# Kernel tuning notes

Measured on AMD Instinct MI355X. Metric: run time of the kernel, lower is better.

## Reference

```python
import jax, jax.numpy as jnp
import numpy as np

B, NR, NT, NUM_ITER = 8192, 128, 64, 64


def setup_inputs() -> dict:
    key = jax.random.key(0)
    k1, k2, k3, k4 = jax.random.split(key, 4)
    Ht = jax.random.normal(k1, (B, NR, NT), dtype=jnp.float32) / np.sqrt(NR)
    yt = jax.random.normal(k2, (B, NR), dtype=jnp.float32)
    sigmat0 = jax.random.uniform(k3, (B,), dtype=jnp.float32) * 0.5 + 0.05
    # prior probabilities alpha[:,0] after slicing; keep strictly in (0,1)
    alpha = 0.2 + 0.6 * jax.random.uniform(k4, (NT,), dtype=jnp.float32)
    taui = jnp.ones((NUM_ITER,), dtype=jnp.float32)   # per-layer taui weights
    delta = jnp.full((NUM_ITER,), 0.1, dtype=jnp.float32)  # per-layer step sizes
    return {"yt": yt, "Ht": Ht, "sigmat0": sigmat0, "alpha": alpha,
            "taui": taui, "delta": delta}


def _cmd_step(s, c, HH, yH, sig2, taui_i, delta_i, t_x):
    # t_x is the temperature used inside tanh for xt (1.0 on the first layer,
    # |taui_i| otherwise); grad_x always uses |taui_i| as in the original code.
    taui_abs = jnp.abs(taui_i)
    xt = jnp.tanh((c + s) * 0.5 * t_x)                      # [B, NT]
    xHH = jnp.einsum('bn,bnm->bm', xt, HH)                  # [B, NT]
    grad_L = sig2 * jnp.tanh(s * 0.5) + 0.5 * taui_abs * (1.0 - xt ** 2) * (xHH - yH)
    return s - delta_i * grad_L


def reference(yt, Ht, sigmat0, alpha, taui, delta):
    # Precompute Gram matrix and matched filter output
    HH = jnp.einsum('brn,brm->bnm', Ht, Ht)                 # [B, NT, NT]
    yH = jnp.einsum('br,brn->bn', yt, Ht)                   # [B, NT]
    c = jnp.log(1.0 / alpha - 1.0)                          # [NT], prior offset
    sig2 = (sigmat0 ** 2)[:, None]                          # [B, 1]
    s0 = jnp.zeros_like(yH)                                 # [B, NT]

    # first layer: xt temperature fixed to 1 (first_iter=True)
    s = _cmd_step(s0, c, HH, yH, sig2, taui[0], delta[0], jnp.float32(1.0))

    def body(s, td):
        taui_i, delta_i = td
        s = _cmd_step(s, c, HH, yH, sig2, taui_i, delta_i, jnp.abs(taui_i))
        return s, None

    s, _ = jax.lax.scan(body, s, (taui[1:], delta[1:]))

    # final soft estimate uses the last layer's taui
    xt = jnp.tanh((c + s) * 0.5 * jnp.abs(taui[-1]))        # [B, NT]
    xt2 = xt[..., None]
    # m == [-1, 1] branch: ft = [P(m=-1), P(m=+1)]
    ft = jnp.concatenate([(1.0 - xt2) * 0.5, (1.0 + xt2) * 0.5], axis=-1)  # [B, NT, 2]
    return ft, xt
```

## Files before the change

kernel.cpp:

```cpp
#include <hip/hip_runtime.h>
#include <hip/hip_bf16.h>


typedef __attribute__((ext_vector_type(8))) short bf16x8;
typedef __attribute__((ext_vector_type(4))) float f32x4;
typedef __attribute__((ext_vector_type(2))) float f32x2;
typedef __attribute__((ext_vector_type(4))) int i32x4;
typedef __attribute__((ext_vector_type(2))) int i32x2;

union FragCast { i32x4 i; bf16x8 h; };

#define NTc 64
#define NRc 128

__device__ __forceinline__ float tanh_fast(float x) {
  float u = __builtin_amdgcn_exp2f(x * 2.88539008177792681f);
  return 1.0f - 2.0f * __builtin_amdgcn_rcpf(u + 1.0f);
}

__device__ __forceinline__ f32x2 pkfma(f32x2 a, f32x2 b, f32x2 c) {
#if __has_builtin(__builtin_elementwise_fma)
  return __builtin_elementwise_fma(a, b, c);
#else
  return c + a * b;
#endif
}

__device__ __forceinline__ float rdlane(float v, int lane) {
  return __int_as_float(__builtin_amdgcn_readlane(__float_as_int(v), lane));
}

__device__ __forceinline__ float partner32(float v, int l) {
#if __has_builtin(__builtin_amdgcn_permlane32_swap)
  i32x2 r = __builtin_amdgcn_permlane32_swap(__float_as_int(v),
                                             __float_as_int(v), false, false);
  return __int_as_float((l & 32) ? r.x : r.y);
#else
  return __shfl_xor(v, 32);
#endif
}

__device__ __forceinline__ float partner16(float v, int l) {
#if __has_builtin(__builtin_amdgcn_permlane16_swap)
  i32x2 r = __builtin_amdgcn_permlane16_swap(__float_as_int(v),
                                             __float_as_int(v), false, false);
  return __int_as_float((l & 16) ? r.x : r.y);
#else
  return __int_as_float(__builtin_amdgcn_ds_swizzle(__float_as_int(v), 0x401F));
#endif
}

__device__ __forceinline__ float xreduce(float t0, float t1, float t2,
                                         float t3, int l) {
  const float A0 = t0 + partner32(t2, l);
  const float A1 = t1 + partner32(t3, l);
  return A0 + partner16(A1, l);
}

__global__ __launch_bounds__(256, 4)
void cmdnet_bin_kernel(const float* __restrict__ yt, const float* __restrict__ Ht,
                       const float* __restrict__ sig0, const float* __restrict__ alpha,
                       const float* __restrict__ taui, const float* __restrict__ delta,
                       float* __restrict__ out, int B, int n_iter) {
  __shared__ __align__(16) float s_xt[4][64];

  const int tid = threadIdx.x;
  const int w = tid >> 6;
  const int l = tid & 63;
  const int g = l >> 4;
  const int c = l & 15;
  const int b = blockIdx.x * 4 + w;
  if (b >= B) return;

  const float* __restrict__ Hb = Ht + (size_t)b * (NRc * NTc);
  const float* __restrict__ yb = yt + (size_t)b * NRc;

  f32x4 acc[4][4];
  #pragma unroll
  for (int i = 0; i < 4; i++)
    #pragma unroll
    for (int j = 0; j < 4; j++) acc[i][j] = (f32x4)0.0f;

  float yhp[4] = {0.0f, 0.0f, 0.0f, 0.0f};

  const int base_l = (g * 8) * NTc + c;

  #pragma unroll
  for (int kk = 0; kk < 4; kk++) {
    const float4 ya  = *reinterpret_cast<const float4*>(yb + kk * 32 + g * 8);
    const float4 yb4 = *reinterpret_cast<const float4*>(yb + kk * 32 + g * 8 + 4);
    const float yv[8] = {ya.x, ya.y, ya.z, ya.w, yb4.x, yb4.y, yb4.z, yb4.w};

    FragCast fh[4], fl[4];
    #pragma unroll
    for (int p = 0; p < 4; p++) {
      #pragma unroll
      for (int jj = 0; jj < 4; jj++) {
        float v0 = Hb[base_l + kk * 32 * NTc + (2 * jj) * NTc + p * 16];
        float v1 = Hb[base_l + kk * 32 * NTc + (2 * jj + 1) * NTc + p * 16];
        yhp[p] = fmaf(yv[2 * jj], v0, yhp[p]);
        yhp[p] = fmaf(yv[2 * jj + 1], v1, yhp[p]);
        unsigned b0 = __float_as_uint(v0), b1 = __float_as_uint(v1);
        unsigned h0 = (b0 + 0x8000u) & 0xffff0000u;
        unsigned h1 = (b1 + 0x8000u) & 0xffff0000u;
        float r0 = v0 - __uint_as_float(h0);
        float r1 = v1 - __uint_as_float(h1);
        fh[p].i[jj] = (int)((h0 >> 16) | h1);
        fl[p].i[jj] = (int)(((__float_as_uint(r0) + 0x8000u) >> 16) |
                            ((__float_as_uint(r1) + 0x8000u) & 0xffff0000u));
      }
    }
    #pragma unroll
    for (int p = 0; p < 4; p++) {
      #pragma unroll
      for (int q = 0; q < 4; q++) {
        acc[p][q] = __builtin_amdgcn_mfma_f32_16x16x32_bf16(fh[p].h, fh[q].h, acc[p][q], 0, 0, 0);
        acc[p][q] = __builtin_amdgcn_mfma_f32_16x16x32_bf16(fh[p].h, fl[q].h, acc[p][q], 0, 0, 0);
        acc[p][q] = __builtin_amdgcn_mfma_f32_16x16x32_bf16(fl[p].h, fh[q].h, acc[p][q], 0, 0, 0);
      }
    }
  }

  const bool pb0 = (g & 1) != 0;
  const bool pb1 = (g & 2) != 0;

  #pragma unroll
  for (int i = 0; i < 4; i++) {
    f32x4 a0 = acc[i][0], a1 = acc[i][1], a2 = acc[i][2], a3 = acc[i][3];
    f32x4 s0 = pb0 ? a1 : a0, s1 = pb0 ? a0 : a1;
    f32x4 s2 = pb0 ? a3 : a2, s3 = pb0 ? a2 : a3;
    acc[i][0] = pb1 ? s2 : s0;
    acc[i][1] = pb1 ? s3 : s1;
    acc[i][2] = pb1 ? s0 : s2;
    acc[i][3] = pb1 ? s1 : s3;
  }

  float yH_l;
  {
    float s0 = pb0 ? yhp[1] : yhp[0], s1 = pb0 ? yhp[0] : yhp[1];
    float s2 = pb0 ? yhp[3] : yhp[2], s3 = pb0 ? yhp[2] : yhp[3];
    float t0 = pb1 ? s2 : s0, t1 = pb1 ? s3 : s1;
    float t2 = pb1 ? s0 : s2, t3 = pb1 ? s1 : s3;
    yH_l = xreduce(t0, t1, t2, t3, l);
  }

  const float a_l = alpha[l];
  const float c_l = logf(1.0f / a_l - 1.0f);
  const float sg = sig0[b];
  const float sig2 = sg * sg;

  const int li = (l < n_iter) ? l : 0;
  const float v_th = 0.5f * fabsf(taui[li]);
  const float v_de = delta[li];

  float s = 0.0f;
  float gp = 0.0f;
  float last_th = 0.5f;

  auto iter_body = [&](float th_xt, float th_grad, float de) {
    const float xtv = tanh_fast((c_l + s) * th_xt);
    s_xt[w][l] = xtv;

    f32x2 t0 = {0.f, 0.f}, t1 = {0.f, 0.f}, t2 = {0.f, 0.f}, t3 = {0.f, 0.f};
    #pragma unroll
    for (int i = 0; i < 4; i++) {
      const f32x4 xv = *reinterpret_cast<const f32x4*>(&s_xt[w][i * 16 + g * 4]);
      const f32x2 xlo = xv.xy, xhi = xv.zw;
      t0 = pkfma(xlo, acc[i][0].xy, t0); t0 = pkfma(xhi, acc[i][0].zw, t0);
      t1 = pkfma(xlo, acc[i][1].xy, t1); t1 = pkfma(xhi, acc[i][1].zw, t1);
      t2 = pkfma(xlo, acc[i][2].xy, t2); t2 = pkfma(xhi, acc[i][2].zw, t2);
      t3 = pkfma(xlo, acc[i][3].xy, t3); t3 = pkfma(xhi, acc[i][3].zw, t3);
    }
    const float xHH = xreduce(t0.x + t0.y, t1.x + t1.y,
                              t2.x + t2.y, t3.x + t3.y, l);
    s = s - de * (gp + th_grad * (1.0f - xtv * xtv) * (xHH - yH_l));
    gp = sig2 * tanh_fast(s * 0.5f);
  };

  {
    const float th0 = rdlane(v_th, 0);
    iter_body(0.5f, th0, rdlane(v_de, 0));
    last_th = th0;
  }
  for (int it = 1; it < n_iter; it++) {
    const float thg = rdlane(v_th, it);
    const float de = rdlane(v_de, it);
    iter_body(thg, thg, de);
    last_th = thg;
  }

  const float xtf = tanh_fast((c_l + s) * last_th);
  float2 ft;
  ft.x = 0.5f * (1.0f - xtf);
  ft.y = 0.5f * (1.0f + xtf);
  *reinterpret_cast<float2*>(out + ((size_t)b * NTc + l) * 2) = ft;
  out[(size_t)B * NTc * 2 + (size_t)b * NTc + l] = xtf;
}

extern "C" void kernel_launch(void* const* d_in, const int* in_sizes, int n_in,
                              void* d_out, int out_size, void* d_ws, size_t ws_size,
                              hipStream_t stream) {
  const float* yt    = (const float*)d_in[0];
  const float* Ht    = (const float*)d_in[1];
  const float* sig0  = (const float*)d_in[2];
  const float* alpha = (const float*)d_in[3];
  const float* taui  = (const float*)d_in[4];
  const float* delta = (const float*)d_in[5];
  const int B = in_sizes[2];
  const int n_iter = in_sizes[4];

  const int blocks = (B + 3) / 4;
  hipLaunchKernelGGL(cmdnet_bin_kernel, dim3(blocks), dim3(256), 0, stream,
                     yt, Ht, sig0, alpha, taui, delta, (float*)d_out, B, n_iter);
}
```

Before: 417.8 us.

## Split Gram computation and iteration loop into two kernels via workspace

Splits the fused kernel into a gram_kernel that builds the per-batch Gram matrix and matched-filter output and writes them to workspace, and an iter_kernel that reloads them and runs the iterative update. This lets each phase run with its own occupancy (launch bounds 3 vs 4), separating the memory/MFMA-heavy phase from the latency-bound iteration loop. In exchange it adds a workspace round trip of about 16 KB per batch element and a second launch. If the workspace is too small, it falls back to the fused kernel.

```diff
diff --git a/kernel.cpp b/kernel.cpp
--- a/kernel.cpp
+++ b/kernel.cpp
@@ -12,6 +12,7 @@
 
 #define NTc 64
 #define NRc 128
+#define WS_BSTRIDE 4160
 
 __device__ __forceinline__ float tanh_fast(float x) {
   float u = __builtin_amdgcn_exp2f(x * 2.88539008177792681f);
@@ -57,32 +58,16 @@
   return A0 + partner16(A1, l);
 }
 
-__global__ __launch_bounds__(256, 4)
-void cmdnet_bin_kernel(const float* __restrict__ yt, const float* __restrict__ Ht,
-                       const float* __restrict__ sig0, const float* __restrict__ alpha,
-                       const float* __restrict__ taui, const float* __restrict__ delta,
-                       float* __restrict__ out, int B, int n_iter) {
-  __shared__ __align__(16) float s_xt[4][64];
-
-  const int tid = threadIdx.x;
-  const int w = tid >> 6;
-  const int l = tid & 63;
-  const int g = l >> 4;
-  const int c = l & 15;
-  const int b = blockIdx.x * 4 + w;
-  if (b >= B) return;
-
-  const float* __restrict__ Hb = Ht + (size_t)b * (NRc * NTc);
-  const float* __restrict__ yb = yt + (size_t)b * NRc;
-
-  f32x4 acc[4][4];
+__device__ __forceinline__ void gram_compute(const float* __restrict__ Hb,
+                                             const float* __restrict__ yb,
+                                             int l, int g, int c,
+                                             f32x4 (&acc)[4][4], float& yH_l) {
   #pragma unroll
   for (int i = 0; i < 4; i++)
     #pragma unroll
     for (int j = 0; j < 4; j++) acc[i][j] = (f32x4)0.0f;
 
   float yhp[4] = {0.0f, 0.0f, 0.0f, 0.0f};
-
   const int base_l = (g * 8) * NTc + c;
 
   #pragma unroll
@@ -135,7 +120,6 @@
     acc[i][3] = pb1 ? s1 : s3;
   }
 
-  float yH_l;
   {
     float s0 = pb0 ? yhp[1] : yhp[0], s1 = pb0 ? yhp[0] : yhp[1];
     float s2 = pb0 ? yhp[3] : yhp[2], s3 = pb0 ? yhp[2] : yhp[3];
@@ -143,6 +127,52 @@
     float t2 = pb1 ? s0 : s2, t3 = pb1 ? s1 : s3;
     yH_l = xreduce(t0, t1, t2, t3, l);
   }
+}
+
+__global__ __launch_bounds__(256, 3)
+void gram_kernel(const float* __restrict__ yt, const float* __restrict__ Ht,
+                 float* __restrict__ ws, int B) {
+  const int tid = threadIdx.x;
+  const int w = tid >> 6, l = tid & 63, g = l >> 4, c = l & 15;
+  const int b = blockIdx.x * 4 + w;
+  if (b >= B) return;
+
+  f32x4 acc[4][4];
+  float yH_l;
+  gram_compute(Ht + (size_t)b * (NRc * NTc), yt + (size_t)b * NRc,
+               l, g, c, acc, yH_l);
+
+  float* wb = ws + (size_t)b * WS_BSTRIDE;
+  #pragma unroll
+  for (int i = 0; i < 4; i++)
+    #pragma unroll
+    for (int k = 0; k < 4; k++)
+      *reinterpret_cast<f32x4*>(wb + (i * 4 + k) * 256 + l * 4) = acc[i][k];
+  wb[4096 + l] = yH_l;
+}
+
+__global__ __launch_bounds__(256, 4)
+void iter_kernel(const float* __restrict__ ws, const float* __restrict__ sig0,
+                 const float* __restrict__ alpha, const float* __restrict__ taui,
+                 const float* __restrict__ delta, float* __restrict__ out,
+                 int B, int n_iter) {
+  __shared__ __align__(16) float s_xt[4][64];
+
+  const int tid = threadIdx.x;
+  const int w = tid >> 6, l = tid & 63, g = l >> 4;
+  const int b = blockIdx.x * 4 + w;
+  if (b >= B) return;
+
+  const float* __restrict__ wb = ws + (size_t)b * WS_BSTRIDE;
+
+  f32x4 hh[4][4];
+  #pragma unroll
+  for (int i = 0; i < 4; i++)
+    #pragma unroll
+    for (int k = 0; k < 4; k++)
+      hh[i][k] = *reinterpret_cast<const f32x4*>(wb + (i * 4 + k) * 256 + l * 4);
+
+  const float yH_l = wb[4096 + l];
 
   const float a_l = alpha[l];
   const float c_l = logf(1.0f / a_l - 1.0f);
@@ -153,9 +183,75 @@
   const float v_th = 0.5f * fabsf(taui[li]);
   const float v_de = delta[li];
 
-  float s = 0.0f;
-  float gp = 0.0f;
-  float last_th = 0.5f;
+  float s = 0.0f, gp = 0.0f, last_th = 0.5f;
+
+  auto iter_body = [&](float th_xt, float th_grad, float de) {
+    const float xtv = tanh_fast((c_l + s) * th_xt);
+    s_xt[w][l] = xtv;
+
+    f32x2 t0 = {0.f, 0.f}, t1 = {0.f, 0.f}, t2 = {0.f, 0.f}, t3 = {0.f, 0.f};
+    #pragma unroll
+    for (int i = 0; i < 4; i++) {
+      const f32x4 xv = *reinterpret_cast<const f32x4*>(&s_xt[w][i * 16 + g * 4]);
+      const f32x2 xlo = xv.xy, xhi = xv.zw;
+      t0 = pkfma(xlo, hh[i][0].xy, t0); t0 = pkfma(xhi, hh[i][0].zw, t0);
+      t1 = pkfma(xlo, hh[i][1].xy, t1); t1 = pkfma(xhi, hh[i][1].zw, t1);
+      t2 = pkfma(xlo, hh[i][2].xy, t2); t2 = pkfma(xhi, hh[i][2].zw, t2);
+      t3 = pkfma(xlo, hh[i][3].xy, t3); t3 = pkfma(xhi, hh[i][3].zw, t3);
+    }
+    const float xHH = xreduce(t0.x + t0.y, t1.x + t1.y,
+                              t2.x + t2.y, t3.x + t3.y, l);
+    s = s - de * (gp + th_grad * (1.0f - xtv * xtv) * (xHH - yH_l));
+    gp = sig2 * tanh_fast(s * 0.5f);
+  };
+
+  {
+    const float th0 = rdlane(v_th, 0);
+    iter_body(0.5f, th0, rdlane(v_de, 0));
+    last_th = th0;
+  }
+  for (int it = 1; it < n_iter; it++) {
+    const float thg = rdlane(v_th, it);
+    const float de = rdlane(v_de, it);
+    iter_body(thg, thg, de);
+    last_th = thg;
+  }
+
+  const float xtf = tanh_fast((c_l + s) * last_th);
+  float2 ft;
+  ft.x = 0.5f * (1.0f - xtf);
+  ft.y = 0.5f * (1.0f + xtf);
+  *reinterpret_cast<float2*>(out + ((size_t)b * NTc + l) * 2) = ft;
+  out[(size_t)B * NTc * 2 + (size_t)b * NTc + l] = xtf;
+}
+
+__global__ __launch_bounds__(256, 4)
+void fused_kernel(const float* __restrict__ yt, const float* __restrict__ Ht,
+                  const float* __restrict__ sig0, const float* __restrict__ alpha,
+                  const float* __restrict__ taui, const float* __restrict__ delta,
+                  float* __restrict__ out, int B, int n_iter) {
+  __shared__ __align__(16) float s_xt[4][64];
+
+  const int tid = threadIdx.x;
+  const int w = tid >> 6, l = tid & 63, g = l >> 4, c = l & 15;
+  const int b = blockIdx.x * 4 + w;
+  if (b >= B) return;
+
+  f32x4 acc[4][4];
+  float yH_l;
+  gram_compute(Ht + (size_t)b * (NRc * NTc), yt + (size_t)b * NRc,
+               l, g, c, acc, yH_l);
+
+  const float a_l = alpha[l];
+  const float c_l = logf(1.0f / a_l - 1.0f);
+  const float sg = sig0[b];
+  const float sig2 = sg * sg;
+
+  const int li = (l < n_iter) ? l : 0;
+  const float v_th = 0.5f * fabsf(taui[li]);
+  const float v_de = delta[li];
+
+  float s = 0.0f, gp = 0.0f, last_th = 0.5f;
 
   auto iter_body = [&](float th_xt, float th_grad, float de) {
     const float xtv = tanh_fast((c_l + s) * th_xt);
@@ -210,6 +306,17 @@
   const int n_iter = in_sizes[4];
 
   const int blocks = (B + 3) / 4;
-  hipLaunchKernelGGL(cmdnet_bin_kernel, dim3(blocks), dim3(256), 0, stream,
-                     yt, Ht, sig0, alpha, taui, delta, (float*)d_out, B, n_iter);
-}
+  const size_t ws_needed = (size_t)B * WS_BSTRIDE * sizeof(float);
+
+  if (ws_size >= ws_needed) {
+    hipLaunchKernelGGL(gram_kernel, dim3(blocks), dim3(256), 0, stream,
+                       yt, Ht, (float*)d_ws, B);
+    hipLaunchKernelGGL(iter_kernel, dim3(blocks), dim3(256), 0, stream,
+                       (const float*)d_ws, sig0, alpha, taui, delta,
+                       (float*)d_out, B, n_iter);
+  } else {
+    hipLaunchKernelGGL(fused_kernel, dim3(blocks), dim3(256), 0, stream,
+                       yt, Ht, sig0, alpha, taui, delta, (float*)d_out,
+                       B, n_iter);
+  }
+}
```

Result: slower. 472.5 us (+13.1%).
